# Kernel optimization log

Hardware: AMD Instinct MI355X
Metric: run time of the kernel (lower is better)

## Reference

```python
import jax, jax.numpy as jnp
import numpy as np

B, S, D, DFF = 4, 2048, 1024, 4096
EPS = 1e-5


def layernorm(x, gamma, beta):
    mu = jnp.mean(x, axis=-1, keepdims=True)
    var = jnp.var(x, axis=-1, keepdims=True)
    return (x - mu) * jax.lax.rsqrt(var + EPS) * gamma + beta


def attention(Q, K, V, causal):
    d_k = Q.shape[-1]
    scores = jnp.einsum('bqd,bkd->bqk', Q, K) / jnp.sqrt(jnp.asarray(d_k, Q.dtype))
    if causal:
        q_len, k_len = scores.shape[-2], scores.shape[-1]
        mask = jnp.tril(jnp.ones((q_len, k_len), dtype=bool))
        scores = jnp.where(mask[None], scores, jnp.asarray(-jnp.inf, scores.dtype))
    w = jax.nn.softmax(scores, axis=-1)
    return jnp.einsum('bqk,bkd->bqd', w, V)


def setup_inputs() -> dict:
    key = jax.random.key(0)
    ks = jax.random.split(key, 12)
    sd = 0.02
    return {
        'y': jax.random.normal(ks[0], (B, S, D), jnp.float32),
        'Z': jax.random.normal(ks[1], (B, S, D), jnp.float32),
        'w1': jax.random.normal(ks[2], (D, DFF), jnp.float32) * sd,
        'b1': jnp.zeros((DFF,), jnp.float32),
        'w2': jax.random.normal(ks[3], (DFF, D), jnp.float32) * sd,
        'b2': jnp.zeros((D,), jnp.float32),
        'g1': jnp.ones((D,), jnp.float32), 'beta1': jnp.zeros((D,), jnp.float32),
        'g2': jnp.ones((D,), jnp.float32), 'beta2': jnp.zeros((D,), jnp.float32),
        'g3': jnp.ones((D,), jnp.float32), 'beta3': jnp.zeros((D,), jnp.float32),
    }


def reference(y, Z, w1, b1, w2, b2, g1, beta1, g2, beta2, g3, beta3):
    # masked (causal) self-attention, single head over full d_model
    sa = attention(y, y, y, causal=True)
    y = layernorm(y + sa, g1, beta1)
    # cross-attention to encoder memory Z
    ca = attention(y, Z, Z, causal=False)
    y = layernorm(y + ca, g2, beta2)
    # position-wise FFN
    h = jax.nn.relu(jnp.einsum('bsd,df->bsf', y, w1) + b1)
    ff = jnp.einsum('bsf,fd->bsd', h, w2) + b2
    y = layernorm(y + ff, g3, beta3)
    return y
```

## Files before the change

### kernel.cpp

```cpp
#include <hip/hip_runtime.h>
#include <hip/hip_bf16.h>
#include <hip/hip_fp8.h>


#define Bb 4
#define Ss 2048
#define Dd 1024
#define Ff 4096

typedef __attribute__((ext_vector_type(4))) float f32x4;
typedef __attribute__((ext_vector_type(8))) short bf16x8;
typedef __attribute__((ext_vector_type(2))) long i64x2;
typedef __attribute__((ext_vector_type(8))) unsigned short u16x8;
typedef __attribute__((ext_vector_type(4))) unsigned short u16x4;

__device__ __forceinline__ unsigned short f2bf(float f) {
  unsigned u = __float_as_uint(f);
  u += 0x7FFFu + ((u >> 16) & 1u);
  return (unsigned short)(u >> 16);
}
__device__ __forceinline__ float bf2f(unsigned short h) {
  return __uint_as_float(((unsigned)h) << 16);
}
__device__ __forceinline__ unsigned char f2f8(float f) {
  __hip_fp8_e4m3 q(f);
  return q.__x;
}
__device__ __forceinline__ int f8col(int c) {
  int g = c >> 6, b = c & 63, o = b >> 3, j = b & 7;
  return g * 64 + (2 * (o & 3) + (o >> 2)) * 8 + j;
}

__device__ __forceinline__ void gload_lds16(const void* g, void* l) {
  __builtin_amdgcn_global_load_lds((const __attribute__((address_space(1))) void*)g,
                                   (__attribute__((address_space(3))) void*)l, 16, 0, 0);
}

__device__ __forceinline__ int xcd8(int orig, int n) {
  int q = n >> 3, r = n & 7;
  int x = orig & 7;
  int base = x < r ? x * (q + 1) : r * (q + 1) + (x - r) * q;
  return base + (orig >> 3);
}

__global__ __launch_bounds__(256) void k_transpose_cast(const float* __restrict__ in,
                                                        unsigned short* __restrict__ outT,
                                                        unsigned char* __restrict__ out8,
                                                        int R, int C) {
  __shared__ float t[32][33];
  size_t bo = (size_t)blockIdx.z * R * C;
  const float* pin = in + bo;
  unsigned short* poutT = outT + bo;
  unsigned char* pout8 = out8 ? out8 + bo : nullptr;
  int c0 = blockIdx.x * 32, r0 = blockIdx.y * 32;
  int tx = threadIdx.x, ty = threadIdx.y;
#pragma unroll
  for (int i = 0; i < 4; i++) {
    float v = pin[(size_t)(r0 + ty + i * 8) * C + c0 + tx];
    t[ty + i * 8][tx] = v;
    if (pout8) pout8[(size_t)(r0 + ty + i * 8) * C + f8col(c0 + tx)] = f2f8(v);
  }
  __syncthreads();
#pragma unroll
  for (int i = 0; i < 4; i++)
    poutT[(size_t)(c0 + ty + i * 8) * R + r0 + tx] = f2bf(t[tx][ty + i * 8]);
}

#define BAR() __builtin_amdgcn_s_barrier()
#define PRIO1() __builtin_amdgcn_s_setprio(1)
#define PRIO0() __builtin_amdgcn_s_setprio(0)

#define LDA8(arr, mh, bo)                                                       \
  {                                                                             \
    _Pragma("unroll") for (int j_ = 0; j_ < QM; ++j_) {                         \
      _Pragma("unroll") for (int kh_ = 0; kh_ < 2; ++kh_) {                     \
        arr[j_][kh_] =                                                          \
            *(const bf16x8*)(lds + (bo) + ((mh)*QM + j_) * 2048 + aof[kh_]);    \
      }                                                                         \
    }                                                                           \
  }

#define LDB8(arr, nh, bo)                                                       \
  {                                                                             \
    _Pragma("unroll") for (int n_ = 0; n_ < 2; ++n_) {                          \
      _Pragma("unroll") for (int kh_ = 0; kh_ < 2; ++kh_) {                     \
        arr[n_][kh_] =                                                          \
            *(const bf16x8*)(lds + (bo) + ((nh)*2 + n_) * 2048 + bof[kh_]);     \
      }                                                                         \
    }                                                                           \
  }

#define MMQ(aarr, barr, mh, nh)                                                 \
  {                                                                             \
    _Pragma("unroll") for (int j_ = 0; j_ < QM; ++j_) {                         \
      _Pragma("unroll") for (int n_ = 0; n_ < 2; ++n_) {                        \
        _Pragma("unroll") for (int kh_ = 0; kh_ < 2; ++kh_) {                   \
          acc[(mh)*QM + j_][(nh)*2 + n_] = __builtin_amdgcn_mfma_f32_16x16x32_bf16( \
              aarr[j_][kh_], barr[n_][kh_], acc[(mh)*QM + j_][(nh)*2 + n_], 0, 0, 0); \
        }                                                                       \
      }                                                                         \
    }                                                                           \
  }

#define LDAF8(arr, mh, bo)                                                      \
  {                                                                             \
    _Pragma("unroll") for (int j_ = 0; j_ < 4; ++j_)                            \
        arr[j_] = *(const i64x2*)(lds + (bo) + ((mh)*4 + j_) * 1024 + aofs);    \
  }
#define LDBF8(arr, nh, bo)                                                      \
  {                                                                             \
    _Pragma("unroll") for (int n_ = 0; n_ < 2; ++n_)                            \
        arr[n_] = *(const i64x2*)(lds + (bo) + ((nh)*2 + n_) * 1024 + bofs);    \
  }
#define MMQF8(aarr, barr, mh, nh)                                               \
  {                                                                             \
    _Pragma("unroll") for (int j_ = 0; j_ < 4; ++j_) {                          \
      _Pragma("unroll") for (int n_ = 0; n_ < 2; ++n_) {                        \
        _Pragma("unroll") for (int kh_ = 0; kh_ < 2; ++kh_) {                   \
          acc[(mh)*4 + j_][(nh)*2 + n_] = __builtin_amdgcn_mfma_f32_16x16x32_fp8_fp8( \
              aarr[j_][kh_], barr[n_][kh_], acc[(mh)*4 + j_][(nh)*2 + n_], 0, 0, 0);  \
        }                                                                       \
      }                                                                         \
    }                                                                           \
  }

#define EPILOGUE(MR_, WMS_)                                                     \
  {                                                                             \
    const int colb = j0 + wc * 64 + fr;                                         \
    const int rowb = i0 + wr * (WMS_) + (kq << 2);                              \
    const size_t cb = (size_t)bz * bsC;                                         \
    _Pragma("unroll") for (int m = 0; m < (MR_); ++m) {                         \
      _Pragma("unroll") for (int r = 0; r < 4; ++r) {                           \
        size_t ro = cb + (size_t)(rowb + m * 16 + r) * ldc;                     \
        _Pragma("unroll") for (int n = 0; n < 4; ++n) {                         \
          float v = acc[m][n][r];                                               \
          int col = colb + n * 16;                                              \
          if (EPI == 0) Cb[ro + col] = f2bf(v * scale);                         \
          else if (EPI == 2) Cb[ro + col] = f2bf(fmaxf(v + bias[col], 0.f));    \
          else if (EPI == 4) Cb[ro + col] = f2bf(v + resid[ro + col]);          \
          else Cb[ro + col] = f2bf(v + bias[col] + resid[ro + col]);            \
        }                                                                       \
      }                                                                         \
    }                                                                           \
  }

template <bool CAUSAL>
__global__ __launch_bounds__(512) void k_gemm8f8(
    const unsigned char* __restrict__ Ag, const unsigned char* __restrict__ Bg,
    unsigned short* __restrict__ Cb,
    int K, int lda, int ldb, int ldc, long bsA, long bsB, long bsC, float scale) {
  constexpr int ABYTES = 16384, BBYTES = 16384;
  __shared__ alignas(16) char lds[2 * ABYTES + 2 * BBYTES];

  int i0, j0;
  if (CAUSAL) {
    int t = xcd8(blockIdx.x, gridDim.x);
    int ti = (int)((sqrtf(8.f * t + 1.f) - 1.f) * 0.5f);
    while ((ti + 1) * (ti + 2) / 2 <= t) ++ti;
    while (ti * (ti + 1) / 2 > t) --ti;
    i0 = ti * 256;
    j0 = (t - ti * (ti + 1) / 2) * 256;
  } else {
    int lin = xcd8(blockIdx.y * gridDim.x + blockIdx.x, gridDim.x * gridDim.y);
    i0 = (lin / gridDim.x) * 256;
    j0 = (lin % gridDim.x) * 256;
  }
  int bz = blockIdx.z;
  Ag += (size_t)bz * bsA;
  Bg += (size_t)bz * bsB;

  const int nk = K / 64;
  const int niter = nk / 2;

  const int tid = threadIdx.x;
  const int w = tid >> 6, lane = tid & 63;
  const int wr = w >> 2, wc = w & 3;

  const int srow = tid >> 2;
  const int scs = (tid & 3) ^ ((tid >> 3) & 3);
  const unsigned char* As = Ag + (size_t)(i0 + srow) * lda + scs * 16;
  const unsigned char* Bs = Bg + (size_t)(j0 + srow) * ldb + scs * 16;

  auto stA = [&](int kt, int hf) {
    int ks = kt < nk ? kt : nk - 1;
    gload_lds16(As + (size_t)(hf * 128) * lda + ks * 64,
                lds + (kt & 1) * ABYTES + hf * 8192 + w * 1024);
  };
  auto stB = [&](int kt, int hf) {
    int ks = kt < nk ? kt : nk - 1;
    gload_lds16(Bs + (size_t)(hf * 128) * ldb + ks * 64,
                lds + 2 * ABYTES + (kt & 1) * BBYTES + hf * 8192 + w * 1024);
  };

  const int fr = lane & 15, kq = lane >> 4;
  const int rA = wr * 128 + fr;
  const int rB = wc * 64 + fr;
  const unsigned aofs = rA * 64 + ((kq ^ ((rA >> 1) & 3)) << 4);
  const unsigned bofs = rB * 64 + ((kq ^ ((rB >> 1) & 3)) << 4);
  constexpr int A0 = 0, A1 = ABYTES, B0 = 2 * ABYTES, B1 = 2 * ABYTES + BBYTES;

  f32x4 acc[8][4];
#pragma unroll
  for (int m = 0; m < 8; ++m)
#pragma unroll
    for (int n = 0; n < 4; ++n) acc[m][n] = (f32x4){0.f, 0.f, 0.f, 0.f};

  i64x2 a0[4], a1[4], b0[2], b1[2];

  stA(0, 0); stA(0, 1); stB(0, 0); stB(0, 1);
  stA(1, 0); stA(1, 1); stB(1, 0);
  asm volatile("s_waitcnt vmcnt(3)" ::: "memory");
  BAR();
  LDAF8(a0, 0, A0); LDBF8(b0, 0, B0);

  for (int t = 0; t < niter; ++t) {
    const int ka = 2 * t + 2, kb = 2 * t + 3;
    LDAF8(a1, 1, A0);
    stB(2 * t + 1, 1);
    BAR(); PRIO1(); MMQF8(a0, b0, 0, 0); PRIO0(); BAR();
    LDBF8(b1, 1, B0);
    stA(ka, 0);
    BAR(); PRIO1(); MMQF8(a1, b0, 1, 0); PRIO0(); BAR();
    stA(ka, 1);
    BAR(); PRIO1(); MMQF8(a0, b1, 0, 1); PRIO0(); BAR();
    stB(ka, 0);
    asm volatile("s_waitcnt vmcnt(3)" ::: "memory");
    BAR();
    LDAF8(a0, 0, A1); LDBF8(b0, 0, B1);
    PRIO1(); MMQF8(a1, b1, 1, 1); PRIO0(); BAR();
    LDAF8(a1, 1, A1);
    stB(ka, 1);
    BAR(); PRIO1(); MMQF8(a0, b0, 0, 0); PRIO0(); BAR();
    LDBF8(b1, 1, B1);
    stA(kb, 0);
    BAR(); PRIO1(); MMQF8(a1, b0, 1, 0); PRIO0(); BAR();
    stA(kb, 1);
    BAR(); PRIO1(); MMQF8(a0, b1, 0, 1); PRIO0(); BAR();
    stB(kb, 0);
    asm volatile("s_waitcnt vmcnt(3)" ::: "memory");
    BAR();
    LDAF8(a0, 0, A0); LDBF8(b0, 0, B0);
    PRIO1(); MMQF8(a1, b1, 1, 1); PRIO0(); BAR();
  }

  const int colb = j0 + wc * 64 + fr;
  const int rowb = i0 + wr * 128 + (kq << 2);
  const size_t cb = (size_t)bz * bsC;
#pragma unroll
  for (int m = 0; m < 8; ++m) {
#pragma unroll
    for (int r = 0; r < 4; ++r) {
      size_t ro = cb + (size_t)(rowb + m * 16 + r) * ldc;
#pragma unroll
      for (int n = 0; n < 4; ++n)
        Cb[ro + colb + n * 16] = f2bf(acc[m][n][r] * scale);
    }
  }
}

template <int EPI, bool CAUSAL>
__global__ __launch_bounds__(512) void k_gemm8(
    const unsigned short* __restrict__ Ag, const unsigned short* __restrict__ Bg,
    unsigned short* __restrict__ Cb,
    const float* __restrict__ bias, const float* __restrict__ resid,
    int K, int lda, int ldb, int ldc, long bsA, long bsB, long bsC, float scale) {
  constexpr int QM = 4;
  constexpr int ABYTES = 32768, BBYTES = 32768;
  __shared__ alignas(16) char lds[2 * ABYTES + 2 * BBYTES];

  int i0, j0;
  if (CAUSAL) {
    int t = xcd8(blockIdx.x, gridDim.x);
    int ti = (int)((sqrtf(8.f * t + 1.f) - 1.f) * 0.5f);
    while ((ti + 1) * (ti + 2) / 2 <= t) ++ti;
    while (ti * (ti + 1) / 2 > t) --ti;
    i0 = ti * 256;
    j0 = (t - ti * (ti + 1) / 2) * 256;
  } else {
    int lin = xcd8(blockIdx.y * gridDim.x + blockIdx.x, gridDim.x * gridDim.y);
    i0 = (lin / gridDim.x) * 256;
    j0 = (lin % gridDim.x) * 256;
  }
  int bz = blockIdx.z;
  Ag += (size_t)bz * bsA;
  Bg += (size_t)bz * bsB;

  const int nk = K / 64;
  const int niter = nk / 2;

  const int tid = threadIdx.x;
  const int w = tid >> 6, lane = tid & 63;
  const int wr = w >> 2, wc = w & 3;

  const int srow = (w << 3) + (lane >> 3);
  const int bcs = (lane & 7) ^ (lane >> 3);
  const unsigned short* As = Ag + (size_t)(i0 + srow) * lda + bcs * 8;
  const unsigned short* Bs = Bg + (size_t)(j0 + srow) * ldb + bcs * 8;
  char* ldsAw = lds + w * 1024;
  char* ldsBw = lds + 2 * ABYTES + w * 1024;

  auto stA = [&](int kt, int hf) {
    int ks = kt < nk ? kt : nk - 1;
#pragma unroll
    for (int l = 0; l < 2; ++l)
      gload_lds16(As + (size_t)(hf * 128 + l * 64) * lda + ks * 64,
                  ldsAw + (kt & 1) * ABYTES + hf * 128 * 128 + l * 8192);
  };
  auto stB = [&](int kt, int hf) {
    int ks = kt < nk ? kt : nk - 1;
#pragma unroll
    for (int l = 0; l < 2; ++l)
      gload_lds16(Bs + (size_t)(hf * 128 + l * 64) * ldb + ks * 64,
                  ldsBw + (kt & 1) * BBYTES + hf * 128 * 128 + l * 8192);
  };

  const int fr = lane & 15, kq = lane >> 4;
  const int rA = wr * 128 + fr;
  const int rB = wc * 64 + fr;
  unsigned aof[2], bof[2];
  aof[0] = rA * 128 + ((kq ^ (rA & 7)) << 4);
  aof[1] = rA * 128 + (((kq + 4) ^ (rA & 7)) << 4);
  bof[0] = 2 * ABYTES + rB * 128 + ((kq ^ (rB & 7)) << 4);
  bof[1] = 2 * ABYTES + rB * 128 + (((kq + 4) ^ (rB & 7)) << 4);
  constexpr int A0 = 0, A1 = ABYTES, B0 = 0, B1 = BBYTES;

  f32x4 acc[8][4];
#pragma unroll
  for (int m = 0; m < 8; ++m)
#pragma unroll
    for (int n = 0; n < 4; ++n) acc[m][n] = (f32x4){0.f, 0.f, 0.f, 0.f};

  bf16x8 a0[QM][2], a1[QM][2], b0[2][2], b1[2][2];

  stA(0, 0); stA(0, 1); stB(0, 0); stB(0, 1);
  stA(1, 0); stA(1, 1); stB(1, 0);
  asm volatile("s_waitcnt vmcnt(6)" ::: "memory");
  BAR();
  LDA8(a0, 0, A0); LDB8(b0, 0, B0);

  for (int t = 0; t < niter; ++t) {
    const int ka = 2 * t + 2, kb = 2 * t + 3;
    LDA8(a1, 1, A0);
    stB(2 * t + 1, 1);
    BAR(); PRIO1(); MMQ(a0, b0, 0, 0); PRIO0(); BAR();
    LDB8(b1, 1, B0);
    stA(ka, 0);
    BAR(); PRIO1(); MMQ(a1, b0, 1, 0); PRIO0(); BAR();
    stA(ka, 1);
    BAR(); PRIO1(); MMQ(a0, b1, 0, 1); PRIO0(); BAR();
    stB(ka, 0);
    asm volatile("s_waitcnt vmcnt(6)" ::: "memory");
    BAR();
    LDA8(a0, 0, A1); LDB8(b0, 0, B1);
    PRIO1(); MMQ(a1, b1, 1, 1); PRIO0(); BAR();
    LDA8(a1, 1, A1);
    stB(ka, 1);
    BAR(); PRIO1(); MMQ(a0, b0, 0, 0); PRIO0(); BAR();
    LDB8(b1, 1, B1);
    stA(kb, 0);
    BAR(); PRIO1(); MMQ(a1, b0, 1, 0); PRIO0(); BAR();
    stA(kb, 1);
    BAR(); PRIO1(); MMQ(a0, b1, 0, 1); PRIO0(); BAR();
    stB(kb, 0);
    asm volatile("s_waitcnt vmcnt(6)" ::: "memory");
    BAR();
    LDA8(a0, 0, A0); LDB8(b0, 0, B0);
    PRIO1(); MMQ(a1, b1, 1, 1); PRIO0(); BAR();
  }
  EPILOGUE(8, 128)
}

template <int EPI, bool KCAP>
__global__ __launch_bounds__(512) void k_gemm4(
    const unsigned short* __restrict__ Ag, const unsigned short* __restrict__ Bg,
    unsigned short* __restrict__ Cb,
    const float* __restrict__ bias, const float* __restrict__ resid,
    int K, int lda, int ldb, int ldc, long bsA, long bsB, long bsC, float scale) {
  constexpr int QM = 4;
  constexpr int ABYTES = 16384, BBYTES = 32768;
  __shared__ alignas(16) char lds[2 * ABYTES + 2 * BBYTES];

  int lin = xcd8(blockIdx.y * gridDim.x + blockIdx.x, gridDim.x * gridDim.y);
  int i0 = (lin / gridDim.x) * 128;
  int j0 = (lin % gridDim.x) * 256;
  int bz = blockIdx.z;
  Ag += (size_t)bz * bsA;
  Bg += (size_t)bz * bsB;

  int nk = K / 64;
  if (KCAP) {
    int cap = i0 / 64 + 2;
    nk = nk < cap ? nk : cap;
  }
  const int niter = nk / 2;

  const int tid = threadIdx.x;
  const int w = tid >> 6, lane = tid & 63;
  const int wr = w >> 2, wc = w & 3;

  const int srow = (w << 3) + (lane >> 3);
  const int bcs = (lane & 7) ^ (lane >> 3);
  const unsigned short* As = Ag + (size_t)(i0 + srow) * lda + bcs * 8;
  const unsigned short* Bs = Bg + (size_t)(j0 + srow) * ldb + bcs * 8;
  char* ldsAw = lds + w * 1024;
  char* ldsBw = lds + 2 * ABYTES + w * 1024;

  auto stA2 = [&](int kt) {
    int ks = kt < nk ? kt : nk - 1;
#pragma unroll
    for (int hf = 0; hf < 2; ++hf)
      gload_lds16(As + (size_t)(hf * 64) * lda + ks * 64,
                  ldsAw + (kt & 1) * ABYTES + hf * 64 * 128);
  };
  auto stBh = [&](int kt, int hf) {
    int ks = kt < nk ? kt : nk - 1;
#pragma unroll
    for (int l = 0; l < 2; ++l)
      gload_lds16(Bs + (size_t)(hf * 128 + l * 64) * ldb + ks * 64,
                  ldsBw + (kt & 1) * BBYTES + hf * 128 * 128 + l * 8192);
  };

  const int fr = lane & 15, kq = lane >> 4;
  const int rA = wr * 64 + fr;
  const int rB = wc * 64 + fr;
  unsigned aof[2], bof[2];
  aof[0] = rA * 128 + ((kq ^ (rA & 7)) << 4);
  aof[1] = rA * 128 + (((kq + 4) ^ (rA & 7)) << 4);
  bof[0] = 2 * ABYTES + rB * 128 + ((kq ^ (rB & 7)) << 4);
  bof[1] = 2 * ABYTES + rB * 128 + (((kq + 4) ^ (rB & 7)) << 4);
  constexpr int A0 = 0, A1 = ABYTES, B0 = 0, B1 = BBYTES;

  f32x4 acc[4][4];
#pragma unroll
  for (int m = 0; m < 4; ++m)
#pragma unroll
    for (int n = 0; n < 4; ++n) acc[m][n] = (f32x4){0.f, 0.f, 0.f, 0.f};

  bf16x8 a[QM][2], b0[2][2], b1[2][2];

  stA2(0); stBh(0, 0); stBh(0, 1);
  stA2(1); stBh(1, 0);
  asm volatile("s_waitcnt vmcnt(4)" ::: "memory");
  BAR();
  LDA8(a, 0, A0); LDB8(b0, 0, B0);

  for (int t = 0; t < niter; ++t) {
    const int ka = 2 * t + 2, kb = 2 * t + 3;
    LDB8(b1, 1, B0);
    stBh(2 * t + 1, 1);
    BAR(); PRIO1(); MMQ(a, b0, 0, 0); PRIO0(); BAR();
    stA2(ka); stBh(ka, 0);
    asm volatile("s_waitcnt vmcnt(4)" ::: "memory");
    BAR();
    PRIO1(); MMQ(a, b1, 0, 1); PRIO0();
    LDA8(a, 0, A1); LDB8(b0, 0, B1);
    BAR();
    LDB8(b1, 1, B1);
    stBh(ka, 1);
    BAR(); PRIO1(); MMQ(a, b0, 0, 0); PRIO0(); BAR();
    stA2(kb); stBh(kb, 0);
    asm volatile("s_waitcnt vmcnt(4)" ::: "memory");
    BAR();
    PRIO1(); MMQ(a, b1, 0, 1); PRIO0();
    LDA8(a, 0, A0); LDB8(b0, 0, B0);
    BAR();
  }
  EPILOGUE(4, 64)
}

template <bool CAUSAL>
__global__ __launch_bounds__(256) void k_softmax(unsigned short* __restrict__ scores) {
  int row = blockIdx.x;
  int i = row & (Ss - 1);
  unsigned short* src = scores + (size_t)row * Ss;
  int nv = CAUSAL ? i + 1 : Ss;
  int nb = CAUSAL ? ((i & ~127) + 128) : Ss;
  int t = threadIdx.x;
  int w = t >> 6, lane = t & 63;
  bool act = t * 8 < nb;
  float v[8];
  float mx = -1e30f;
  if (act) {
    u16x8 raw = *(const u16x8*)(src + t * 8);
#pragma unroll
    for (int k = 0; k < 8; k++) {
      int j = t * 8 + k;
      v[k] = (j < nv) ? bf2f(raw[k]) : -1e30f;
      mx = fmaxf(mx, v[k]);
    }
  } else {
#pragma unroll
    for (int k = 0; k < 8; k++) v[k] = -1e30f;
  }
#pragma unroll
  for (int o = 32; o; o >>= 1) mx = fmaxf(mx, __shfl_xor(mx, o));
  __shared__ float red[8];
  if (lane == 0) red[w] = mx;
  __syncthreads();
  mx = fmaxf(fmaxf(red[0], red[1]), fmaxf(red[2], red[3]));
  float sum = 0.f;
#pragma unroll
  for (int k = 0; k < 8; k++) {
    float e = (v[k] > -1e29f) ? __expf(v[k] - mx) : 0.f;
    v[k] = e;
    sum += e;
  }
#pragma unroll
  for (int o = 32; o; o >>= 1) sum += __shfl_xor(sum, o);
  if (lane == 0) red[4 + w] = sum;
  __syncthreads();
  sum = red[4] + red[5] + red[6] + red[7];
  float inv = 1.f / sum;
  if (act) {
    u16x8 r;
#pragma unroll
    for (int k = 0; k < 8; k++) r[k] = f2bf(v[k] * inv);
    *(u16x8*)(src + t * 8) = r;
  }
}

template <int OM>
__global__ __launch_bounds__(256) void k_ln(const unsigned short* __restrict__ a,
                                            const float* __restrict__ g,
                                            const float* __restrict__ be,
                                            float* __restrict__ outf,
                                            unsigned short* __restrict__ outb,
                                            unsigned char* __restrict__ out8) {
  int row = blockIdx.x;
  size_t o = (size_t)row * Dd;
  int t = threadIdx.x;
  u16x4 raw = *(const u16x4*)(a + o + t * 4);
  f32x4 x;
#pragma unroll
  for (int k = 0; k < 4; k++) x[k] = bf2f(raw[k]);
  float s = x[0] + x[1] + x[2] + x[3];
  float q = x[0] * x[0] + x[1] * x[1] + x[2] * x[2] + x[3] * x[3];
  int w = t >> 6, lane = t & 63;
#pragma unroll
  for (int of = 32; of; of >>= 1) {
    s += __shfl_xor(s, of);
    q += __shfl_xor(q, of);
  }
  __shared__ float red[8];
  if (lane == 0) {
    red[w] = s;
    red[4 + w] = q;
  }
  __syncthreads();
  s = red[0] + red[1] + red[2] + red[3];
  q = red[4] + red[5] + red[6] + red[7];
  float mean = s * (1.f / Dd);
  float var = q * (1.f / Dd) - mean * mean;
  float rstd = rsqrtf(var + 1e-5f);
  f32x4 gv = *(const f32x4*)(g + t * 4);
  f32x4 bv = *(const f32x4*)(be + t * 4);
  f32x4 y;
#pragma unroll
  for (int k = 0; k < 4; k++) y[k] = (x[k] - mean) * rstd * gv[k] + bv[k];
  *(f32x4*)(outf + o + t * 4) = y;
  if (OM == 1) {
    u16x4 r;
    r[0] = f2bf(y[0]); r[1] = f2bf(y[1]); r[2] = f2bf(y[2]); r[3] = f2bf(y[3]);
    *(u16x4*)(outb + o + t * 4) = r;
  } else if (OM == 2) {
    int cbyte = t * 4;
    int gq = cbyte >> 6, oo = (cbyte >> 3) & 7, j = cbyte & 7;
    int phys = gq * 64 + (2 * (oo & 3) + (oo >> 2)) * 8 + j;
    unsigned r = (unsigned)f2f8(y[0]) | ((unsigned)f2f8(y[1]) << 8) |
                 ((unsigned)f2f8(y[2]) << 16) | ((unsigned)f2f8(y[3]) << 24);
    *(unsigned*)(out8 + (size_t)row * Dd + phys) = r;
  }
}

extern "C" void kernel_launch(void* const* d_in, const int* in_sizes, int n_in, void* d_out,
                              int out_size, void* d_ws, size_t ws_size, hipStream_t stream) {
  (void)in_sizes; (void)n_in; (void)out_size; (void)ws_size;
  const float* y   = (const float*)d_in[0];
  const float* Z   = (const float*)d_in[1];
  const float* w1  = (const float*)d_in[2];
  const float* b1  = (const float*)d_in[3];
  const float* w2  = (const float*)d_in[4];
  const float* b2  = (const float*)d_in[5];
  const float* g1  = (const float*)d_in[6];
  const float* be1 = (const float*)d_in[7];
  const float* g2  = (const float*)d_in[8];
  const float* be2 = (const float*)d_in[9];
  const float* g3  = (const float*)d_in[10];
  const float* be3 = (const float*)d_in[11];
  float* out = (float*)d_out;

  char* ws = (char*)d_ws;
  const size_t MB = 1024ull * 1024ull;
  unsigned short* T   = (unsigned short*)(ws);
  unsigned short* Zt  = (unsigned short*)(ws + 16 * MB);
  unsigned short* ybf = (unsigned short*)(ws + 32 * MB);
  unsigned short* w1t = (unsigned short*)(ws + 48 * MB);
  unsigned short* w2t = (unsigned short*)(ws + 56 * MB);
  unsigned short* sc  = (unsigned short*)(ws + 64 * MB);
  unsigned short* h   = (unsigned short*)(ws + 64 * MB);
  unsigned char* y8   = (unsigned char*)(ws + 96 * MB);
  unsigned char* Z8   = (unsigned char*)(ws + 104 * MB);
  unsigned char* y18  = (unsigned char*)(ws + 112 * MB);
  float* res          = (float*)(ws + 128 * MB);
  unsigned short* attnb = (unsigned short*)d_out;

  dim3 b256(256), b512(512);
  const float scl = 1.f / 32.f;
  const long SD = (long)Ss * Dd, SS = (long)Ss * Ss;

  k_transpose_cast<<<dim3(Dd / 32, Ss / 32, Bb), dim3(32, 8), 0, stream>>>(y, T, y8, Ss, Dd);
  k_transpose_cast<<<dim3(Dd / 32, Ss / 32, Bb), dim3(32, 8), 0, stream>>>(Z, Zt, Z8, Ss, Dd);
  k_transpose_cast<<<dim3(Ff / 32, Dd / 32, 1), dim3(32, 8), 0, stream>>>(w1, w1t, nullptr, Dd, Ff);
  k_transpose_cast<<<dim3(Dd / 32, Ff / 32, 1), dim3(32, 8), 0, stream>>>(w2, w2t, nullptr, Ff, Dd);

  k_gemm8f8<true><<<dim3(36, 1, Bb), b512, 0, stream>>>(
      y8, y8, sc, Dd, Dd, Dd, Ss, SD, SD, SS, scl);
  k_softmax<true><<<dim3(Bb * Ss), b256, 0, stream>>>(sc);
  k_gemm4<4, true><<<dim3(Dd / 256, Ss / 128, Bb), b512, 0, stream>>>(
      sc, T, attnb, nullptr, y, Ss, Ss, Ss, Dd, SS, SD, SD, 1.f);
  k_ln<2><<<dim3(Bb * Ss), b256, 0, stream>>>(attnb, g1, be1, res, nullptr, y18);

  k_gemm8f8<false><<<dim3(Ss / 256, Ss / 256, Bb), b512, 0, stream>>>(
      y18, Z8, sc, Dd, Dd, Dd, Ss, SD, SD, SS, scl);
  k_softmax<false><<<dim3(Bb * Ss), b256, 0, stream>>>(sc);
  k_gemm4<4, false><<<dim3(Dd / 256, Ss / 128, Bb), b512, 0, stream>>>(
      sc, Zt, attnb, nullptr, res, Ss, Ss, Ss, Dd, SS, SD, SD, 1.f);
  k_ln<1><<<dim3(Bb * Ss), b256, 0, stream>>>(attnb, g2, be2, res, ybf, nullptr);

  k_gemm8<2, false><<<dim3(Ff / 256, (Bb * Ss) / 256, 1), b512, 0, stream>>>(
      ybf, w1t, h, b1, nullptr, Dd, Dd, Dd, Ff, 0L, 0L, 0L, 1.f);
  k_gemm4<5, false><<<dim3(Dd / 256, (Bb * Ss) / 128, 1), b512, 0, stream>>>(
      h, w2t, T, b2, res, Ff, Ff, Ff, Dd, 0L, 0L, 0L, 1.f);
  k_ln<0><<<dim3(Bb * Ss), b256, 0, stream>>>(T, g3, be3, out, nullptr, nullptr);
}
```

Measured before the change: 367.1 us.

## Restructure GEMM main loops: merged MFMA phases and triple-buffered LDS for 128-row GEMM

The 256x256 bf16 and fp8 GEMMs now issue two MFMA quadrants per barrier phase instead of one. Their fragment loads move to the start of each half-iteration, which halves the barrier count per k-step. The 128x256 GEMM switches to a simple per-k-tile loop with three LDS stages, prefetching two tiles ahead, and one barrier pair per tile. The aim is to cut synchronization overhead and improve the overlap of memory with compute. The cost is more live fragment registers and more LDS (144KB for the triple-buffered kernel), which may reduce occupancy or scheduling freedom.

```diff
diff --git a/kernel.cpp b/kernel.cpp
--- a/kernel.cpp
+++ b/kernel.cpp
@@ -144,12 +144,14 @@
     }                                                                           \
   }
 
-template <bool CAUSAL>
-__global__ __launch_bounds__(512) void k_gemm8f8(
-    const unsigned char* __restrict__ Ag, const unsigned char* __restrict__ Bg,
+template <int EPI, bool CAUSAL>
+__global__ __launch_bounds__(512) void k_gemm8m(
+    const unsigned short* __restrict__ Ag, const unsigned short* __restrict__ Bg,
     unsigned short* __restrict__ Cb,
+    const float* __restrict__ bias, const float* __restrict__ resid,
     int K, int lda, int ldb, int ldc, long bsA, long bsB, long bsC, float scale) {
-  constexpr int ABYTES = 16384, BBYTES = 16384;
+  constexpr int QM = 4;
+  constexpr int ABYTES = 32768, BBYTES = 32768;
   __shared__ alignas(16) char lds[2 * ABYTES + 2 * BBYTES];
 
   int i0, j0;
@@ -176,28 +178,37 @@
   const int w = tid >> 6, lane = tid & 63;
   const int wr = w >> 2, wc = w & 3;
 
-  const int srow = tid >> 2;
-  const int scs = (tid & 3) ^ ((tid >> 3) & 3);
-  const unsigned char* As = Ag + (size_t)(i0 + srow) * lda + scs * 16;
-  const unsigned char* Bs = Bg + (size_t)(j0 + srow) * ldb + scs * 16;
+  const int srow = (w << 3) + (lane >> 3);
+  const int bcs = (lane & 7) ^ (lane >> 3);
+  const unsigned short* As = Ag + (size_t)(i0 + srow) * lda + bcs * 8;
+  const unsigned short* Bs = Bg + (size_t)(j0 + srow) * ldb + bcs * 8;
+  char* ldsAw = lds + w * 1024;
+  char* ldsBw = lds + 2 * ABYTES + w * 1024;
 
   auto stA = [&](int kt, int hf) {
     int ks = kt < nk ? kt : nk - 1;
-    gload_lds16(As + (size_t)(hf * 128) * lda + ks * 64,
-                lds + (kt & 1) * ABYTES + hf * 8192 + w * 1024);
+#pragma unroll
+    for (int l = 0; l < 2; ++l)
+      gload_lds16(As + (size_t)(hf * 128 + l * 64) * lda + ks * 64,
+                  ldsAw + (kt & 1) * ABYTES + hf * 128 * 128 + l * 8192);
   };
   auto stB = [&](int kt, int hf) {
     int ks = kt < nk ? kt : nk - 1;
-    gload_lds16(Bs + (size_t)(hf * 128) * ldb + ks * 64,
-                lds + 2 * ABYTES + (kt & 1) * BBYTES + hf * 8192 + w * 1024);
+#pragma unroll
+    for (int l = 0; l < 2; ++l)
+      gload_lds16(Bs + (size_t)(hf * 128 + l * 64) * ldb + ks * 64,
+                  ldsBw + (kt & 1) * BBYTES + hf * 128 * 128 + l * 8192);
   };
 
   const int fr = lane & 15, kq = lane >> 4;
   const int rA = wr * 128 + fr;
   const int rB = wc * 64 + fr;
-  const unsigned aofs = rA * 64 + ((kq ^ ((rA >> 1) & 3)) << 4);
-  const unsigned bofs = rB * 64 + ((kq ^ ((rB >> 1) & 3)) << 4);
-  constexpr int A0 = 0, A1 = ABYTES, B0 = 2 * ABYTES, B1 = 2 * ABYTES + BBYTES;
+  unsigned aof[2], bof[2];
+  aof[0] = rA * 128 + ((kq ^ (rA & 7)) << 4);
+  aof[1] = rA * 128 + (((kq + 4) ^ (rA & 7)) << 4);
+  bof[0] = 2 * ABYTES + rB * 128 + ((kq ^ (rB & 7)) << 4);
+  bof[1] = 2 * ABYTES + rB * 128 + (((kq + 4) ^ (rB & 7)) << 4);
+  constexpr int A0 = 0, A1 = ABYTES, B0 = 0, B1 = BBYTES;
 
   f32x4 acc[8][4];
 #pragma unroll
@@ -205,67 +216,39 @@
 #pragma unroll
     for (int n = 0; n < 4; ++n) acc[m][n] = (f32x4){0.f, 0.f, 0.f, 0.f};
 
-  i64x2 a0[4], a1[4], b0[2], b1[2];
+  bf16x8 a0[QM][2], a1[QM][2], b0[2][2], b1[2][2];
 
   stA(0, 0); stA(0, 1); stB(0, 0); stB(0, 1);
   stA(1, 0); stA(1, 1); stB(1, 0);
-  asm volatile("s_waitcnt vmcnt(3)" ::: "memory");
+  asm volatile("s_waitcnt vmcnt(6)" ::: "memory");
   BAR();
-  LDAF8(a0, 0, A0); LDBF8(b0, 0, B0);
 
   for (int t = 0; t < niter; ++t) {
     const int ka = 2 * t + 2, kb = 2 * t + 3;
-    LDAF8(a1, 1, A0);
+    LDA8(a0, 0, A0); LDA8(a1, 1, A0); LDB8(b0, 0, B0);
     stB(2 * t + 1, 1);
-    BAR(); PRIO1(); MMQF8(a0, b0, 0, 0); PRIO0(); BAR();
-    LDBF8(b1, 1, B0);
-    stA(ka, 0);
-    BAR(); PRIO1(); MMQF8(a1, b0, 1, 0); PRIO0(); BAR();
-    stA(ka, 1);
-    BAR(); PRIO1(); MMQF8(a0, b1, 0, 1); PRIO0(); BAR();
-    stB(ka, 0);
-    asm volatile("s_waitcnt vmcnt(3)" ::: "memory");
-    BAR();
-    LDAF8(a0, 0, A1); LDBF8(b0, 0, B1);
-    PRIO1(); MMQF8(a1, b1, 1, 1); PRIO0(); BAR();
-    LDAF8(a1, 1, A1);
+    BAR(); PRIO1(); MMQ(a0, b0, 0, 0); MMQ(a1, b0, 1, 0); PRIO0(); BAR();
+    LDB8(b1, 1, B0);
+    stA(ka, 0); stA(ka, 1); stB(ka, 0);
+    asm volatile("s_waitcnt vmcnt(6)" ::: "memory");
+    BAR(); PRIO1(); MMQ(a1, b1, 1, 1); MMQ(a0, b1, 0, 1); PRIO0(); BAR();
+    LDA8(a0, 0, A1); LDA8(a1, 1, A1); LDB8(b0, 0, B1);
     stB(ka, 1);
-    BAR(); PRIO1(); MMQF8(a0, b0, 0, 0); PRIO0(); BAR();
-    LDBF8(b1, 1, B1);
-    stA(kb, 0);
-    BAR(); PRIO1(); MMQF8(a1, b0, 1, 0); PRIO0(); BAR();
-    stA(kb, 1);
-    BAR(); PRIO1(); MMQF8(a0, b1, 0, 1); PRIO0(); BAR();
-    stB(kb, 0);
-    asm volatile("s_waitcnt vmcnt(3)" ::: "memory");
-    BAR();
-    LDAF8(a0, 0, A0); LDBF8(b0, 0, B0);
-    PRIO1(); MMQF8(a1, b1, 1, 1); PRIO0(); BAR();
-  }
-
-  const int colb = j0 + wc * 64 + fr;
-  const int rowb = i0 + wr * 128 + (kq << 2);
-  const size_t cb = (size_t)bz * bsC;
-#pragma unroll
-  for (int m = 0; m < 8; ++m) {
-#pragma unroll
-    for (int r = 0; r < 4; ++r) {
-      size_t ro = cb + (size_t)(rowb + m * 16 + r) * ldc;
-#pragma unroll
-      for (int n = 0; n < 4; ++n)
-        Cb[ro + colb + n * 16] = f2bf(acc[m][n][r] * scale);
-    }
-  }
-}
-
-template <int EPI, bool CAUSAL>
-__global__ __launch_bounds__(512) void k_gemm8(
-    const unsigned short* __restrict__ Ag, const unsigned short* __restrict__ Bg,
+    BAR(); PRIO1(); MMQ(a0, b0, 0, 0); MMQ(a1, b0, 1, 0); PRIO0(); BAR();
+    LDB8(b1, 1, B1);
+    stA(kb, 0); stA(kb, 1); stB(kb, 0);
+    asm volatile("s_waitcnt vmcnt(6)" ::: "memory");
+    BAR(); PRIO1(); MMQ(a1, b1, 1, 1); MMQ(a0, b1, 0, 1); PRIO0(); BAR();
+  }
+  EPILOGUE(8, 128)
+}
+
+template <bool CAUSAL>
+__global__ __launch_bounds__(512) void k_gemm8f8m(
+    const unsigned char* __restrict__ Ag, const unsigned char* __restrict__ Bg,
     unsigned short* __restrict__ Cb,
-    const float* __restrict__ bias, const float* __restrict__ resid,
     int K, int lda, int ldb, int ldc, long bsA, long bsB, long bsC, float scale) {
-  constexpr int QM = 4;
-  constexpr int ABYTES = 32768, BBYTES = 32768;
+  constexpr int ABYTES = 16384, BBYTES = 16384;
   __shared__ alignas(16) char lds[2 * ABYTES + 2 * BBYTES];
 
   int i0, j0;
@@ -292,37 +275,28 @@
   const int w = tid >> 6, lane = tid & 63;
   const int wr = w >> 2, wc = w & 3;
 
-  const int srow = (w << 3) + (lane >> 3);
-  const int bcs = (lane & 7) ^ (lane >> 3);
-  const unsigned short* As = Ag + (size_t)(i0 + srow) * lda + bcs * 8;
-  const unsigned short* Bs = Bg + (size_t)(j0 + srow) * ldb + bcs * 8;
-  char* ldsAw = lds + w * 1024;
-  char* ldsBw = lds + 2 * ABYTES + w * 1024;
+  const int srow = tid >> 2;
+  const int scs = (tid & 3) ^ ((tid >> 3) & 3);
+  const unsigned char* As = Ag + (size_t)(i0 + srow) * lda + scs * 16;
+  const unsigned char* Bs = Bg + (size_t)(j0 + srow) * ldb + scs * 16;
 
   auto stA = [&](int kt, int hf) {
     int ks = kt < nk ? kt : nk - 1;
-#pragma unroll
-    for (int l = 0; l < 2; ++l)
-      gload_lds16(As + (size_t)(hf * 128 + l * 64) * lda + ks * 64,
-                  ldsAw + (kt & 1) * ABYTES + hf * 128 * 128 + l * 8192);
+    gload_lds16(As + (size_t)(hf * 128) * lda + ks * 64,
+                lds + (kt & 1) * ABYTES + hf * 8192 + w * 1024);
   };
   auto stB = [&](int kt, int hf) {
     int ks = kt < nk ? kt : nk - 1;
-#pragma unroll
-    for (int l = 0; l < 2; ++l)
-      gload_lds16(Bs + (size_t)(hf * 128 + l * 64) * ldb + ks * 64,
-                  ldsBw + (kt & 1) * BBYTES + hf * 128 * 128 + l * 8192);
+    gload_lds16(Bs + (size_t)(hf * 128) * ldb + ks * 64,
+                lds + 2 * ABYTES + (kt & 1) * BBYTES + hf * 8192 + w * 1024);
   };
 
   const int fr = lane & 15, kq = lane >> 4;
   const int rA = wr * 128 + fr;
   const int rB = wc * 64 + fr;
-  unsigned aof[2], bof[2];
-  aof[0] = rA * 128 + ((kq ^ (rA & 7)) << 4);
-  aof[1] = rA * 128 + (((kq + 4) ^ (rA & 7)) << 4);
-  bof[0] = 2 * ABYTES + rB * 128 + ((kq ^ (rB & 7)) << 4);
-  bof[1] = 2 * ABYTES + rB * 128 + (((kq + 4) ^ (rB & 7)) << 4);
-  constexpr int A0 = 0, A1 = ABYTES, B0 = 0, B1 = BBYTES;
+  const unsigned aofs = rA * 64 + ((kq ^ ((rA >> 1) & 3)) << 4);
+  const unsigned bofs = rB * 64 + ((kq ^ ((rB >> 1) & 3)) << 4);
+  constexpr int A0 = 0, A1 = ABYTES, B0 = 2 * ABYTES, B1 = 2 * ABYTES + BBYTES;
 
   f32x4 acc[8][4];
 #pragma unroll
@@ -330,55 +304,55 @@
 #pragma unroll
     for (int n = 0; n < 4; ++n) acc[m][n] = (f32x4){0.f, 0.f, 0.f, 0.f};
 
-  bf16x8 a0[QM][2], a1[QM][2], b0[2][2], b1[2][2];
+  i64x2 a0[4], a1[4], b0[2], b1[2];
 
   stA(0, 0); stA(0, 1); stB(0, 0); stB(0, 1);
   stA(1, 0); stA(1, 1); stB(1, 0);
-  asm volatile("s_waitcnt vmcnt(6)" ::: "memory");
+  asm volatile("s_waitcnt vmcnt(3)" ::: "memory");
   BAR();
-  LDA8(a0, 0, A0); LDB8(b0, 0, B0);
 
   for (int t = 0; t < niter; ++t) {
     const int ka = 2 * t + 2, kb = 2 * t + 3;
-    LDA8(a1, 1, A0);
+    LDAF8(a0, 0, A0); LDAF8(a1, 1, A0); LDBF8(b0, 0, B0);
     stB(2 * t + 1, 1);
-    BAR(); PRIO1(); MMQ(a0, b0, 0, 0); PRIO0(); BAR();
-    LDB8(b1, 1, B0);
-    stA(ka, 0);
-    BAR(); PRIO1(); MMQ(a1, b0, 1, 0); PRIO0(); BAR();
-    stA(ka, 1);
-    BAR(); PRIO1(); MMQ(a0, b1, 0, 1); PRIO0(); BAR();
-    stB(ka, 0);
-    asm volatile("s_waitcnt vmcnt(6)" ::: "memory");
-    BAR();
-    LDA8(a0, 0, A1); LDB8(b0, 0, B1);
-    PRIO1(); MMQ(a1, b1, 1, 1); PRIO0(); BAR();
-    LDA8(a1, 1, A1);
+    BAR(); PRIO1(); MMQF8(a0, b0, 0, 0); MMQF8(a1, b0, 1, 0); PRIO0(); BAR();
+    LDBF8(b1, 1, B0);
+    stA(ka, 0); stA(ka, 1); stB(ka, 0);
+    asm volatile("s_waitcnt vmcnt(3)" ::: "memory");
+    BAR(); PRIO1(); MMQF8(a1, b1, 1, 1); MMQF8(a0, b1, 0, 1); PRIO0(); BAR();
+    LDAF8(a0, 0, A1); LDAF8(a1, 1, A1); LDBF8(b0, 0, B1);
     stB(ka, 1);
-    BAR(); PRIO1(); MMQ(a0, b0, 0, 0); PRIO0(); BAR();
-    LDB8(b1, 1, B1);
-    stA(kb, 0);
-    BAR(); PRIO1(); MMQ(a1, b0, 1, 0); PRIO0(); BAR();
-    stA(kb, 1);
-    BAR(); PRIO1(); MMQ(a0, b1, 0, 1); PRIO0(); BAR();
-    stB(kb, 0);
-    asm volatile("s_waitcnt vmcnt(6)" ::: "memory");
-    BAR();
-    LDA8(a0, 0, A0); LDB8(b0, 0, B0);
-    PRIO1(); MMQ(a1, b1, 1, 1); PRIO0(); BAR();
-  }
-  EPILOGUE(8, 128)
+    BAR(); PRIO1(); MMQF8(a0, b0, 0, 0); MMQF8(a1, b0, 1, 0); PRIO0(); BAR();
+    LDBF8(b1, 1, B1);
+    stA(kb, 0); stA(kb, 1); stB(kb, 0);
+    asm volatile("s_waitcnt vmcnt(3)" ::: "memory");
+    BAR(); PRIO1(); MMQF8(a1, b1, 1, 1); MMQF8(a0, b1, 0, 1); PRIO0(); BAR();
+  }
+
+  const int colb = j0 + wc * 64 + fr;
+  const int rowb = i0 + wr * 128 + (kq << 2);
+  const size_t cb = (size_t)bz * bsC;
+#pragma unroll
+  for (int m = 0; m < 8; ++m) {
+#pragma unroll
+    for (int r = 0; r < 4; ++r) {
+      size_t ro = cb + (size_t)(rowb + m * 16 + r) * ldc;
+#pragma unroll
+      for (int n = 0; n < 4; ++n)
+        Cb[ro + colb + n * 16] = f2bf(acc[m][n][r] * scale);
+    }
+  }
 }
 
 template <int EPI, bool KCAP>
-__global__ __launch_bounds__(512) void k_gemm4(
+__global__ __launch_bounds__(512) void k3(
     const unsigned short* __restrict__ Ag, const unsigned short* __restrict__ Bg,
     unsigned short* __restrict__ Cb,
     const float* __restrict__ bias, const float* __restrict__ resid,
     int K, int lda, int ldb, int ldc, long bsA, long bsB, long bsC, float scale) {
   constexpr int QM = 4;
-  constexpr int ABYTES = 16384, BBYTES = 32768;
-  __shared__ alignas(16) char lds[2 * ABYTES + 2 * BBYTES];
+  constexpr int ABY = 16384, BBY = 32768, TBY = ABY + BBY;
+  __shared__ alignas(16) char lds[3 * TBY];
 
   int lin = xcd8(blockIdx.y * gridDim.x + blockIdx.x, gridDim.x * gridDim.y);
   int i0 = (lin / gridDim.x) * 128;
@@ -392,32 +366,24 @@
     int cap = i0 / 64 + 2;
     nk = nk < cap ? nk : cap;
   }
-  const int niter = nk / 2;
 
   const int tid = threadIdx.x;
   const int w = tid >> 6, lane = tid & 63;
   const int wr = w >> 2, wc = w & 3;
 
-  const int srow = (w << 3) + (lane >> 3);
-  const int bcs = (lane & 7) ^ (lane >> 3);
+  const int srow = tid >> 3;
+  const int bcs = (tid & 7) ^ (srow & 7);
   const unsigned short* As = Ag + (size_t)(i0 + srow) * lda + bcs * 8;
   const unsigned short* Bs = Bg + (size_t)(j0 + srow) * ldb + bcs * 8;
-  char* ldsAw = lds + w * 1024;
-  char* ldsBw = lds + 2 * ABYTES + w * 1024;
-
-  auto stA2 = [&](int kt) {
+
+  auto stage = [&](int kt, char* dst) {
     int ks = kt < nk ? kt : nk - 1;
 #pragma unroll
-    for (int hf = 0; hf < 2; ++hf)
-      gload_lds16(As + (size_t)(hf * 64) * lda + ks * 64,
-                  ldsAw + (kt & 1) * ABYTES + hf * 64 * 128);
-  };
-  auto stBh = [&](int kt, int hf) {
-    int ks = kt < nk ? kt : nk - 1;
-#pragma unroll
-    for (int l = 0; l < 2; ++l)
-      gload_lds16(Bs + (size_t)(hf * 128 + l * 64) * ldb + ks * 64,
-                  ldsBw + (kt & 1) * BBYTES + hf * 128 * 128 + l * 8192);
+    for (int i = 0; i < 2; ++i)
+      gload_lds16(As + (size_t)(i * 64) * lda + ks * 64, dst + i * 8192 + w * 1024);
+#pragma unroll
+    for (int i = 0; i < 4; ++i)
+      gload_lds16(Bs + (size_t)(i * 64) * ldb + ks * 64, dst + ABY + i * 8192 + w * 1024);
   };
 
   const int fr = lane & 15, kq = lane >> 4;
@@ -426,9 +392,8 @@
   unsigned aof[2], bof[2];
   aof[0] = rA * 128 + ((kq ^ (rA & 7)) << 4);
   aof[1] = rA * 128 + (((kq + 4) ^ (rA & 7)) << 4);
-  bof[0] = 2 * ABYTES + rB * 128 + ((kq ^ (rB & 7)) << 4);
-  bof[1] = 2 * ABYTES + rB * 128 + (((kq + 4) ^ (rB & 7)) << 4);
-  constexpr int A0 = 0, A1 = ABYTES, B0 = 0, B1 = BBYTES;
+  bof[0] = ABY + rB * 128 + ((kq ^ (rB & 7)) << 4);
+  bof[1] = ABY + rB * 128 + (((kq + 4) ^ (rB & 7)) << 4);
 
   f32x4 acc[4][4];
 #pragma unroll
@@ -438,32 +403,35 @@
 
   bf16x8 a[QM][2], b0[2][2], b1[2][2];
 
-  stA2(0); stBh(0, 0); stBh(0, 1);
-  stA2(1); stBh(1, 0);
-  asm volatile("s_waitcnt vmcnt(4)" ::: "memory");
+  stage(0, lds);
+  stage(1, lds + TBY);
+  asm volatile("s_waitcnt vmcnt(6)" ::: "memory");
   BAR();
-  LDA8(a, 0, A0); LDB8(b0, 0, B0);
-
-  for (int t = 0; t < niter; ++t) {
-    const int ka = 2 * t + 2, kb = 2 * t + 3;
-    LDB8(b1, 1, B0);
-    stBh(2 * t + 1, 1);
-    BAR(); PRIO1(); MMQ(a, b0, 0, 0); PRIO0(); BAR();
-    stA2(ka); stBh(ka, 0);
-    asm volatile("s_waitcnt vmcnt(4)" ::: "memory");
+
+  int c = 0, cn = 2;
+  for (int kt = 0; kt < nk; ++kt) {
+    const char* buf = lds + c * TBY;
+#pragma unroll
+    for (int j_ = 0; j_ < QM; ++j_)
+#pragma unroll
+      for (int kh_ = 0; kh_ < 2; ++kh_)
+        a[j_][kh_] = *(const bf16x8*)(buf + j_ * 2048 + aof[kh_]);
+#pragma unroll
+    for (int n_ = 0; n_ < 2; ++n_)
+#pragma unroll
+      for (int kh_ = 0; kh_ < 2; ++kh_) {
+        b0[n_][kh_] = *(const bf16x8*)(buf + n_ * 2048 + bof[kh_]);
+        b1[n_][kh_] = *(const bf16x8*)(buf + (2 + n_) * 2048 + bof[kh_]);
+      }
+    stage(kt + 2, lds + cn * TBY);
+    asm volatile("s_waitcnt vmcnt(6)" ::: "memory");
     BAR();
-    PRIO1(); MMQ(a, b1, 0, 1); PRIO0();
-    LDA8(a, 0, A1); LDB8(b0, 0, B1);
+    PRIO1();
+    MMQ(a, b0, 0, 0); MMQ(a, b1, 0, 1);
+    PRIO0();
     BAR();
-    LDB8(b1, 1, B1);
-    stBh(ka, 1);
-    BAR(); PRIO1(); MMQ(a, b0, 0, 0); PRIO0(); BAR();
-    stA2(kb); stBh(kb, 0);
-    asm volatile("s_waitcnt vmcnt(4)" ::: "memory");
-    BAR();
-    PRIO1(); MMQ(a, b1, 0, 1); PRIO0();
-    LDA8(a, 0, A0); LDB8(b0, 0, B0);
-    BAR();
+    c = (c == 2) ? 0 : c + 1;
+    cn = (cn == 2) ? 0 : cn + 1;
   }
   EPILOGUE(4, 64)
 }
@@ -613,23 +581,23 @@
   k_transpose_cast<<<dim3(Ff / 32, Dd / 32, 1), dim3(32, 8), 0, stream>>>(w1, w1t, nullptr, Dd, Ff);
   k_transpose_cast<<<dim3(Dd / 32, Ff / 32, 1), dim3(32, 8), 0, stream>>>(w2, w2t, nullptr, Ff, Dd);
 
-  k_gemm8f8<true><<<dim3(36, 1, Bb), b512, 0, stream>>>(
+  k_gemm8f8m<true><<<dim3(36, 1, Bb), b512, 0, stream>>>(
       y8, y8, sc, Dd, Dd, Dd, Ss, SD, SD, SS, scl);
   k_softmax<true><<<dim3(Bb * Ss), b256, 0, stream>>>(sc);
-  k_gemm4<4, true><<<dim3(Dd / 256, Ss / 128, Bb), b512, 0, stream>>>(
+  k3<4, true><<<dim3(Dd / 256, Ss / 128, Bb), b512, 0, stream>>>(
       sc, T, attnb, nullptr, y, Ss, Ss, Ss, Dd, SS, SD, SD, 1.f);
   k_ln<2><<<dim3(Bb * Ss), b256, 0, stream>>>(attnb, g1, be1, res, nullptr, y18);
 
-  k_gemm8f8<false><<<dim3(Ss / 256, Ss / 256, Bb), b512, 0, stream>>>(
+  k_gemm8f8m<false><<<dim3(Ss / 256, Ss / 256, Bb), b512, 0, stream>>>(
       y18, Z8, sc, Dd, Dd, Dd, Ss, SD, SD, SS, scl);
   k_softmax<false><<<dim3(Bb * Ss), b256, 0, stream>>>(sc);
-  k_gemm4<4, false><<<dim3(Dd / 256, Ss / 128, Bb), b512, 0, stream>>>(
+  k3<4, false><<<dim3(Dd / 256, Ss / 128, Bb), b512, 0, stream>>>(
       sc, Zt, attnb, nullptr, res, Ss, Ss, Ss, Dd, SS, SD, SD, 1.f);
   k_ln<1><<<dim3(Bb * Ss), b256, 0, stream>>>(attnb, g2, be2, res, ybf, nullptr);
 
-  k_gemm8<2, false><<<dim3(Ff / 256, (Bb * Ss) / 256, 1), b512, 0, stream>>>(
+  k_gemm8m<2, false><<<dim3(Ff / 256, (Bb * Ss) / 256, 1), b512, 0, stream>>>(
       ybf, w1t, h, b1, nullptr, Dd, Dd, Dd, Ff, 0L, 0L, 0L, 1.f);
-  k_gemm4<5, false><<<dim3(Dd / 256, (Bb * Ss) / 128, 1), b512, 0, stream>>>(
+  k3<5, false><<<dim3(Dd / 256, (Bb * Ss) / 128, 1), b512, 0, stream>>>(
       h, w2t, T, b2, res, Ff, Ff, Ff, Dd, 0L, 0L, 0L, 1.f);
   k_ln<0><<<dim3(Bb * Ss), b256, 0, stream>>>(T, g3, be3, out, nullptr, nullptr);
 }
```

Measured after the change: 380.2 us. 3.6% more time.
